# Optimization experiments

Hardware: AMD Instinct MI355X
Metric: run time of the kernel (lower is better)

Reference implementation:

```python
import jax, jax.numpy as jnp
import numpy as np

B, S, D = 2, 2048, 1024
H = 16
HD = D // H  # 64
FORESIGHT = -1e9  # masked_fill value for non-causal positions


def setup_inputs() -> dict:
    key = jax.random.key(0)
    ks = jax.random.split(key, 8)
    s = 0.02
    return {
        "x": jax.random.normal(ks[0], (B, S, D), dtype=jnp.float32),
        "Wq": jax.random.normal(ks[1], (D, H * HD), dtype=jnp.float32) * s,
        "bq": jax.random.normal(ks[2], (H * HD,), dtype=jnp.float32) * s,
        "Wk": jax.random.normal(ks[3], (D, H * HD), dtype=jnp.float32) * s,
        "Wv": jax.random.normal(ks[4], (D, H * HD), dtype=jnp.float32) * s,
        "Wo": jax.random.normal(ks[5], (H * HD, D), dtype=jnp.float32) * s,
        "bo": jax.random.normal(ks[6], (D,), dtype=jnp.float32) * s,
    }


def reference(x, Wq, bq, Wk, Wv, Wo, bo):
    b, s, _ = x.shape
    # projections -> [B, H, S, HD]
    q = (x @ Wq + bq).reshape(b, s, H, HD).transpose(0, 2, 1, 3)
    k = (x @ Wk).reshape(b, s, H, HD).transpose(0, 2, 1, 3)
    v = (x @ Wv).reshape(b, s, H, HD).transpose(0, 2, 1, 3)
    # scores [B, H, S, S]
    scores = jnp.einsum("bhqd,bhkd->bhqk", q, k) / jnp.sqrt(jnp.float32(HD))
    # ALiBi bias: slope_h * j (key position), broadcast over queries
    slopes = 2.0 ** (-8.0 * jnp.arange(1, H + 1, dtype=jnp.float32) / H)
    positions = jnp.arange(s, dtype=jnp.float32)
    scores = scores - slopes[None, :, None, None] * positions[None, None, None, :]
    # causal mask: fill strictly-upper triangle with foresight
    causal = jnp.tril(jnp.ones((s, s), dtype=bool))
    scores = jnp.where(causal[None, None, :, :], scores, FORESIGHT)
    attn = jax.nn.softmax(scores, axis=-1)
    out = jnp.einsum("bhqk,bhkd->bhqd", attn, v)
    out = out.transpose(0, 2, 1, 3).reshape(b, s, H * HD)
    return out @ Wo + bo
```

## Files before the change

### kernel.cpp

```cpp
#include <hip/hip_runtime.h>
#include <stdint.h>

#define DDIM 1024
#define HH 16
#define HDIM 64
#define SS 2048

typedef short bf16x8 __attribute__((ext_vector_type(8)));
typedef float f32x4 __attribute__((ext_vector_type(4)));
typedef float f32x16 __attribute__((ext_vector_type(16)));
typedef unsigned short u16;

__device__ __forceinline__ unsigned f2bf(float f) {
  unsigned u = __builtin_bit_cast(unsigned, f);
  u = u + 0x7FFFu + ((u >> 16) & 1u);
  return u >> 16;
}

__device__ __forceinline__ unsigned cvt_pk_bf16(float a, float b) {
  unsigned r;
  asm("v_cvt_pk_bf16_f32 %0, %1, %2" : "=v"(r) : "v"(a), "v"(b));
  return r;
}

__device__ __forceinline__ void pswap(unsigned& a, unsigned& b) {
  asm volatile("v_permlane32_swap_b32 %0, %1" : "+v"(a), "+v"(b));
}

__device__ __forceinline__ void gload16(const void* g, void* l) {
  __builtin_amdgcn_global_load_lds(
      (const __attribute__((address_space(1))) unsigned int*)g,
      (__attribute__((address_space(3))) unsigned int*)l, 16, 0, 0);
}

__device__ __forceinline__ f32x16 zero16() {
  f32x16 z;
#pragma unroll
  for (int r = 0; r < 16; r++) z[r] = 0.f;
  return z;
}

__global__ void k_convert_x(const float* __restrict__ x, u16* __restrict__ xb) {
  int i = (blockIdx.x * 256 + threadIdx.x) * 4;
  float4 v = *(const float4*)(x + i);
  ushort4 o;
  o.x = (u16)f2bf(v.x); o.y = (u16)f2bf(v.y); o.z = (u16)f2bf(v.z); o.w = (u16)f2bf(v.w);
  *(ushort4*)(xb + i) = o;
}

__global__ void k_transpose_w(const float* __restrict__ w0, const float* __restrict__ w1,
                              const float* __restrict__ w2, const float* __restrict__ w3,
                              u16* __restrict__ wt) {
  __shared__ float t[64][65];
  int z = blockIdx.z;
  const float* src = (z == 0) ? w0 : (z == 1) ? w1 : (z == 2) ? w2 : w3;
  u16* dst = wt + (size_t)z * DDIM * DDIM;
  int k0 = blockIdx.x * 64, n0 = blockIdx.y * 64;
  int tid = threadIdx.x;
  int c4 = tid & 15, rr = tid >> 4;
  for (int rep = 0; rep < 4; rep++) {
    int r = rr + rep * 16;
    float4 v = *(const float4*)(src + (size_t)(k0 + r) * DDIM + n0 + c4 * 4);
    t[r][c4 * 4 + 0] = v.x; t[r][c4 * 4 + 1] = v.y;
    t[r][c4 * 4 + 2] = v.z; t[r][c4 * 4 + 3] = v.w;
  }
  __syncthreads();
  for (int rep = 0; rep < 4; rep++) {
    int n = rr + rep * 16;
    ushort4 o;
    o.x = (u16)f2bf(t[c4 * 4 + 0][n]); o.y = (u16)f2bf(t[c4 * 4 + 1][n]);
    o.z = (u16)f2bf(t[c4 * 4 + 2][n]); o.w = (u16)f2bf(t[c4 * 4 + 3][n]);
    *(ushort4*)(dst + (size_t)(n0 + n) * DDIM + k0 + c4 * 4) = o;
  }
}

template <int MODE>
__global__ __launch_bounds__(256, 2) void k_gemm(const u16* __restrict__ A,
                                                 const u16* __restrict__ BT,
                                                 const float* __restrict__ bias,
                                                 void* __restrict__ O0,
                                                 void* __restrict__ O1,
                                                 void* __restrict__ O2) {
  __shared__ __align__(16) u16 lA[128 * 64];
  __shared__ __align__(16) u16 lB[128 * 64];
  const int tid = threadIdx.x;
  const int l = tid & 63, w = tid >> 6;
  const int wm = w >> 1, wn = w & 1;
  const int m0 = blockIdx.x * 128, n0 = blockIdx.y * 128;
  const int lr = l >> 4, lc = l & 15;

  const int srow = l >> 3;
  const int scol = ((l & 7) ^ srow) * 8;

  f32x4 acc[4][4];
  for (int mi = 0; mi < 4; mi++)
    for (int ni = 0; ni < 4; ni++)
      acc[mi][ni] = f32x4{0.f, 0.f, 0.f, 0.f};

  for (int kk = 0; kk < 16; kk++) {
    const int k0 = kk * 64;
    for (int i = 0; i < 4; i++) {
      int c = w * 4 + i;
      gload16(A + (size_t)(m0 + c * 8 + srow) * DDIM + k0 + scol, (char*)lA + c * 1024);
      gload16(BT + (size_t)(n0 + c * 8 + srow) * DDIM + k0 + scol, (char*)lB + c * 1024);
    }
    __syncthreads();
    for (int ks = 0; ks < 2; ks++) {
      bf16x8 af[4], bfr[4];
      for (int mi = 0; mi < 4; mi++) {
        int row = wm * 64 + mi * 16 + lc;
        int slot = (ks * 4 + lr) ^ (row & 7);
        af[mi] = *(const bf16x8*)((const char*)lA + row * 128 + slot * 16);
      }
      for (int ni = 0; ni < 4; ni++) {
        int row = wn * 64 + ni * 16 + lc;
        int slot = (ks * 4 + lr) ^ (row & 7);
        bfr[ni] = *(const bf16x8*)((const char*)lB + row * 128 + slot * 16);
      }
      for (int mi = 0; mi < 4; mi++)
        for (int ni = 0; ni < 4; ni++)
          acc[mi][ni] = __builtin_amdgcn_mfma_f32_16x16x32_bf16(af[mi], bfr[ni], acc[mi][ni], 0, 0, 0);
    }
    __syncthreads();
  }

  if (MODE == 0) {
    const int which = blockIdx.y >> 3;
    if (which == 0) {
      u16* C = (u16*)O0;
      const float c1 = 0.18033688011112043f;
      for (int mi = 0; mi < 4; mi++)
        for (int ni = 0; ni < 4; ni++) {
          int nl = (n0 + wn * 64 + ni * 16 + lc) & 1023;
          float badd = bias[nl];
          for (int r = 0; r < 4; r++) {
            int m = m0 + wm * 64 + mi * 16 + lr * 4 + r;
            C[(size_t)m * DDIM + nl] = (u16)f2bf((acc[mi][ni][r] + badd) * c1);
          }
        }
    } else if (which == 1) {
      u16* C = (u16*)O1;
      for (int mi = 0; mi < 4; mi++)
        for (int ni = 0; ni < 4; ni++) {
          int nl = (n0 + wn * 64 + ni * 16 + lc) & 1023;
          for (int r = 0; r < 4; r++) {
            int m = m0 + wm * 64 + mi * 16 + lr * 4 + r;
            C[(size_t)m * DDIM + nl] = (u16)f2bf(acc[mi][ni][r]);
          }
        }
    } else {
      u16* C = (u16*)O2;
      for (int mi = 0; mi < 4; mi++)
        for (int ni = 0; ni < 4; ni++) {
          int nl = (n0 + wn * 64 + ni * 16 + lc) & 1023;
          int h = nl >> 6, hd = nl & 63;
          int m = m0 + wm * 64 + mi * 16 + lr * 4;
          int b = m >> 11, s = m & 2047;
          unsigned d0 = f2bf(acc[mi][ni][0]) | (f2bf(acc[mi][ni][1]) << 16);
          unsigned d1 = f2bf(acc[mi][ni][2]) | (f2bf(acc[mi][ni][3]) << 16);
          u16* p = C + ((size_t)((b * HH + h) * HDIM + hd)) * SS + s;
          *(unsigned*)(p) = d0;
          *(unsigned*)(p + 2) = d1;
        }
    }
  } else {
    float* C = (float*)O0;
    for (int mi = 0; mi < 4; mi++)
      for (int ni = 0; ni < 4; ni++) {
        int n = n0 + wn * 64 + ni * 16 + lc;
        float badd = bias[n];
        for (int r = 0; r < 4; r++) {
          int m = m0 + wm * 64 + mi * 16 + lr * 4 + r;
          C[(size_t)m * DDIM + n] = acc[mi][ni][r] + badd;
        }
      }
  }
}

__global__ __launch_bounds__(256, 2) void k_attn(const u16* __restrict__ Q,
                                                 const u16* __restrict__ Kg,
                                                 const u16* __restrict__ Vt,
                                                 u16* __restrict__ AO) {
  __shared__ __align__(16) u16 lK[2][64 * 64];
  __shared__ __align__(16) u16 lV[2][64 * 64];

  const int tid = threadIdx.x;
  const int l = tid & 63, w = tid >> 6;
  const int lq = l & 31, hi = l >> 5;
  const int id = blockIdx.x;
  const int bh = id & 31;
  const int gslot = id >> 5;
  const int g = (gslot < 8) ? gslot : 23 - gslot;
  const int b = bh >> 4, h = bh & 15;
  const int sw = g * 4 + w;
  const int qglob = sw * 32 + lq;
  const int nktw = (sw >> 1) + 1;
  const int nkt = 2 * g + 2;

  const float slope2 = exp2f(-0.5f * (float)(h + 1)) * 1.4426950408889634f;
  const float sh4 = slope2 * (float)(4 * hi);

  f32x16 scr;
#pragma unroll
  for (int r = 0; r < 16; r++) scr[r] = slope2 * (float)((r & 3) + 8 * (r >> 2));

  bf16x8 qf[4];
#pragma unroll
  for (int sd = 0; sd < 4; sd++)
    qf[sd] = *(const bf16x8*)(Q + (size_t)(b * SS + qglob) * DDIM + h * HDIM + sd * 16 + hi * 8);

  f32x16 o0 = zero16(), o1 = zero16();
  float mrun = -3.0e38f, lrl = 0.f;

  const int srow = l >> 3;
  const int scol = ((l & 7) ^ srow) * 8;

  auto stage = [&](int kt, int bb) {
#pragma unroll
    for (int i = 0; i < 2; i++) {
      int c = i * 4 + w;
      gload16(Kg + (size_t)(b * SS + kt * 64 + c * 8 + srow) * DDIM + h * HDIM + scol,
              (char*)lK[bb] + c * 1024);
      gload16(Vt + ((size_t)bh * HDIM + c * 8 + srow) * SS + kt * 64 + scol,
              (char*)lV[bb] + c * 1024);
    }
  };

  stage(0, 0);
  stage(1, 1);

  for (int t = 0; t < nkt; t++) {
    asm volatile("s_waitcnt vmcnt(4)" ::: "memory");
    __builtin_amdgcn_s_barrier();
    asm volatile("" ::: "memory");
    if (t < nktw) {
      const char* Kc = (const char*)lK[t & 1];
      const char* Vc = (const char*)lV[t & 1];
      const bool lastp = (t == nktw - 1);
      const bool doT1 = !lastp || (sw & 1);
      const bool mT0 = lastp && !(sw & 1);
      const bool mT1 = lastp && (sw & 1);

      f32x16 s0 = zero16(), s1 = zero16();
      __builtin_amdgcn_s_setprio(1);
#pragma unroll
      for (int sd = 0; sd < 4; sd++) {
        int row = lq;
        int slot = (2 * sd + hi) ^ (row & 7);
        bf16x8 a = *(const bf16x8*)(Kc + row * 128 + slot * 16);
        s0 = __builtin_amdgcn_mfma_f32_32x32x16_bf16(a, qf[sd], s0, 0, 0, 0);
      }
      if (doT1) {
#pragma unroll
        for (int sd = 0; sd < 4; sd++) {
          int row = 32 + lq;
          int slot = (2 * sd + hi) ^ (row & 7);
          bf16x8 a = *(const bf16x8*)(Kc + row * 128 + slot * 16);
          s1 = __builtin_amdgcn_mfma_f32_32x32x16_bf16(a, qf[sd], s1, 0, 0, 0);
        }
      }
      __builtin_amdgcn_s_setprio(0);

      const float bt0 = -slope2 * (float)(t * 64) - sh4;
      const float bt1 = bt0 - slope2 * 32.f;
      float tmax = -3.0e38f;
#pragma unroll
      for (int r = 0; r < 16; r++) {
        float sv = (s0[r] + bt0) - scr[r];
        if (mT0) {
          int key = t * 64 + (r & 3) + 8 * (r >> 2) + 4 * hi;
          if (key > qglob) sv = -3.0e38f;
        }
        s0[r] = sv;
        tmax = fmaxf(tmax, sv);
      }
      if (doT1) {
#pragma unroll
        for (int r = 0; r < 16; r++) {
          float sv = (s1[r] + bt1) - scr[r];
          if (mT1) {
            int key = t * 64 + 32 + (r & 3) + 8 * (r >> 2) + 4 * hi;
            if (key > qglob) sv = -3.0e38f;
          }
          s1[r] = sv;
          tmax = fmaxf(tmax, sv);
        }
      }
      float tcol = fmaxf(tmax, __shfl_xor(tmax, 32));
      if (__any(tcol > mrun)) {
        float mnew = fmaxf(mrun, tcol);
        float corr = exp2f(mrun - mnew);
        lrl *= corr;
#pragma unroll
        for (int r = 0; r < 16; r++) { o0[r] *= corr; o1[r] *= corr; }
        mrun = mnew;
      }

      f32x4 ps = f32x4{0.f, 0.f, 0.f, 0.f};
#pragma unroll
      for (int r = 0; r < 16; r++) {
        float p = exp2f(s0[r] - mrun);
        s0[r] = p;
        ps[r & 3] += p;
      }
      if (doT1) {
#pragma unroll
        for (int r = 0; r < 16; r++) {
          float p = exp2f(s1[r] - mrun);
          s1[r] = p;
          ps[r & 3] += p;
        }
      }
      lrl += (ps[0] + ps[1]) + (ps[2] + ps[3]);

      __builtin_amdgcn_s_setprio(1);
      auto pvstep = [&](const f32x16& cs, int s) {
        const int b8 = (s & 1) * 8;
        unsigned x1 = cvt_pk_bf16(cs[b8 + 0], cs[b8 + 1]);
        unsigned y1 = cvt_pk_bf16(cs[b8 + 4], cs[b8 + 5]);
        pswap(x1, y1);
        unsigned x2 = cvt_pk_bf16(cs[b8 + 2], cs[b8 + 3]);
        unsigned y2 = cvt_pk_bf16(cs[b8 + 6], cs[b8 + 7]);
        pswap(x2, y2);
        uint4 pw; pw.x = x1; pw.y = x2; pw.z = y1; pw.w = y2;
        bf16x8 pb = __builtin_bit_cast(bf16x8, pw);
        int slotb = 2 * s + hi;
        {
          int row = lq;
          bf16x8 va = *(const bf16x8*)(Vc + row * 128 + ((slotb ^ (row & 7)) << 4));
          o0 = __builtin_amdgcn_mfma_f32_32x32x16_bf16(va, pb, o0, 0, 0, 0);
        }
        {
          int row = 32 + lq;
          bf16x8 va = *(const bf16x8*)(Vc + row * 128 + ((slotb ^ (row & 7)) << 4));
          o1 = __builtin_amdgcn_mfma_f32_32x32x16_bf16(va, pb, o1, 0, 0, 0);
        }
      };
      pvstep(s0, 0);
      pvstep(s0, 1);
      if (doT1) {
        pvstep(s1, 2);
        pvstep(s1, 3);
      }
      __builtin_amdgcn_s_setprio(0);
    }
    __builtin_amdgcn_s_barrier();
    asm volatile("" ::: "memory");
    int kts = t + 2;
    if (kts > nkt - 1) kts = nkt - 1;
    stage(kts, t & 1);
  }

  float lcol = lrl + __shfl_xor(lrl, 32);
  float inv = 1.f / lcol;
  u16* obase = AO + (size_t)(b * SS + qglob) * DDIM + h * HDIM;
#pragma unroll
  for (int rg = 0; rg < 4; rg++) {
    uint2 uu;
    uu.x = cvt_pk_bf16(o0[4 * rg + 0] * inv, o0[4 * rg + 1] * inv);
    uu.y = cvt_pk_bf16(o0[4 * rg + 2] * inv, o0[4 * rg + 3] * inv);
    *(uint2*)(obase + rg * 8 + 4 * hi) = uu;
    uu.x = cvt_pk_bf16(o1[4 * rg + 0] * inv, o1[4 * rg + 1] * inv);
    uu.y = cvt_pk_bf16(o1[4 * rg + 2] * inv, o1[4 * rg + 3] * inv);
    *(uint2*)(obase + 32 + rg * 8 + 4 * hi) = uu;
  }
}

extern "C" void kernel_launch(void* const* d_in, const int* in_sizes, int n_in,
                              void* d_out, int out_size, void* d_ws, size_t ws_size,
                              hipStream_t stream) {
  const float* x  = (const float*)d_in[0];
  const float* Wq = (const float*)d_in[1];
  const float* bq = (const float*)d_in[2];
  const float* Wk = (const float*)d_in[3];
  const float* Wv = (const float*)d_in[4];
  const float* Wo = (const float*)d_in[5];
  const float* bo = (const float*)d_in[6];
  float* out = (float*)d_out;

  u16* ws = (u16*)d_ws;
  const size_t MEG = 1024 * 1024;
  u16* xb = ws;
  u16* WT = ws + 4 * MEG;
  u16* Qb = ws + 8 * MEG;
  u16* Kb = ws + 12 * MEG;
  u16* Vt = ws + 16 * MEG;
  u16* AO = ws + 20 * MEG;

  k_convert_x<<<dim3(4096), dim3(256), 0, stream>>>(x, xb);
  k_transpose_w<<<dim3(16, 16, 4), dim3(256), 0, stream>>>(Wq, Wk, Wv, Wo, WT);
  k_gemm<0><<<dim3(32, 24), dim3(256), 0, stream>>>(xb, WT, bq, (void*)Qb, (void*)Kb, (void*)Vt);
  k_attn<<<dim3(512), dim3(256), 0, stream>>>(Qb, Kb, Vt, AO);
  k_gemm<1><<<dim3(32, 8), dim3(256), 0, stream>>>(AO, WT + 3 * MEG, bo, (void*)out, nullptr, nullptr);
}
```

Measured before the change: 133.6 us.

## Split causal attention along keys into chunks with a separate combine kernel

Attention blocks now each cover one 128-query tile and a chunk of at most eight key tiles, giving 1280 blocks in place of 512 paired blocks. Each block writes its unnormalized fp32 partial output plus running max and sum, and a new combine kernel merges the chunks with rescaled weights before writing bf16. The aim is to balance work across the GPU's compute units and improve occupancy under the causal triangle. The cost is an extra kernel launch, fp32 partial traffic to global memory, and a loop that decodes the block index.

```diff
diff --git a/kernel.cpp b/kernel.cpp
--- a/kernel.cpp
+++ b/kernel.cpp
@@ -177,10 +177,11 @@
   }
 }
 
-__global__ __launch_bounds__(256, 2) void k_attn(const u16* __restrict__ Q,
+__global__ __launch_bounds__(256, 5) void k_attn(const u16* __restrict__ Q,
                                                  const u16* __restrict__ Kg,
                                                  const u16* __restrict__ Vt,
-                                                 u16* __restrict__ AO) {
+                                                 float* __restrict__ Opart,
+                                                 float* __restrict__ Ml) {
   __shared__ __align__(16) u16 lK[2][64 * 64];
   __shared__ __align__(16) u16 lV[2][64 * 64];
 
@@ -189,13 +190,15 @@
   const int lq = l & 31, hi = l >> 5;
   const int id = blockIdx.x;
   const int bh = id & 31;
-  const int gslot = id >> 5;
-  const int g = (gslot < 8) ? gslot : 23 - gslot;
+  int rem = id >> 5, j = 0;
+  while (rem >= 1 + (j >> 2)) { rem -= 1 + (j >> 2); j++; }
+  const int c = rem;
   const int b = bh >> 4, h = bh & 15;
-  const int sw = g * 4 + w;
-  const int qglob = sw * 32 + lq;
-  const int nktw = (sw >> 1) + 1;
-  const int nkt = 2 * g + 2;
+  const int nkt_blk = 2 * j + 2;
+  const int t0 = c * 8;
+  const int t1 = min(t0 + 8, nkt_blk);
+  const int nktw = 2 * j + 1 + (w >> 1);
+  const int qglob = j * 128 + w * 32 + lq;
 
   const float slope2 = exp2f(-0.5f * (float)(h + 1)) * 1.4426950408889634f;
   const float sh4 = slope2 * (float)(4 * hi);
@@ -218,18 +221,18 @@
   auto stage = [&](int kt, int bb) {
 #pragma unroll
     for (int i = 0; i < 2; i++) {
-      int c = i * 4 + w;
-      gload16(Kg + (size_t)(b * SS + kt * 64 + c * 8 + srow) * DDIM + h * HDIM + scol,
-              (char*)lK[bb] + c * 1024);
-      gload16(Vt + ((size_t)bh * HDIM + c * 8 + srow) * SS + kt * 64 + scol,
-              (char*)lV[bb] + c * 1024);
+      int cc = i * 4 + w;
+      gload16(Kg + (size_t)(b * SS + kt * 64 + cc * 8 + srow) * DDIM + h * HDIM + scol,
+              (char*)lK[bb] + cc * 1024);
+      gload16(Vt + ((size_t)bh * HDIM + cc * 8 + srow) * SS + kt * 64 + scol,
+              (char*)lV[bb] + cc * 1024);
     }
   };
 
-  stage(0, 0);
-  stage(1, 1);
-
-  for (int t = 0; t < nkt; t++) {
+  stage(t0, 0);
+  stage(t0 + 1 < t1 ? t0 + 1 : t1 - 1, 1);
+
+  for (int t = t0; t < t1; t++) {
     asm volatile("s_waitcnt vmcnt(4)" ::: "memory");
     __builtin_amdgcn_s_barrier();
     asm volatile("" ::: "memory");
@@ -237,9 +240,9 @@
       const char* Kc = (const char*)lK[t & 1];
       const char* Vc = (const char*)lV[t & 1];
       const bool lastp = (t == nktw - 1);
-      const bool doT1 = !lastp || (sw & 1);
-      const bool mT0 = lastp && !(sw & 1);
-      const bool mT1 = lastp && (sw & 1);
+      const bool doT1 = !lastp || (w & 1);
+      const bool mT0 = lastp && !(w & 1);
+      const bool mT1 = lastp && (w & 1);
 
       f32x16 s0 = zero16(), s1 = zero16();
       __builtin_amdgcn_s_setprio(1);
@@ -347,23 +350,85 @@
     __builtin_amdgcn_s_barrier();
     asm volatile("" ::: "memory");
     int kts = t + 2;
-    if (kts > nkt - 1) kts = nkt - 1;
+    if (kts > t1 - 1) kts = t1 - 1;
     stage(kts, t & 1);
   }
 
   float lcol = lrl + __shfl_xor(lrl, 32);
-  float inv = 1.f / lcol;
-  u16* obase = AO + (size_t)(b * SS + qglob) * DDIM + h * HDIM;
+  float* Op = Opart + (size_t)id * 8192 + (w * 32 + lq) * 64;
 #pragma unroll
   for (int rg = 0; rg < 4; rg++) {
-    uint2 uu;
-    uu.x = cvt_pk_bf16(o0[4 * rg + 0] * inv, o0[4 * rg + 1] * inv);
-    uu.y = cvt_pk_bf16(o0[4 * rg + 2] * inv, o0[4 * rg + 3] * inv);
-    *(uint2*)(obase + rg * 8 + 4 * hi) = uu;
-    uu.x = cvt_pk_bf16(o1[4 * rg + 0] * inv, o1[4 * rg + 1] * inv);
-    uu.y = cvt_pk_bf16(o1[4 * rg + 2] * inv, o1[4 * rg + 3] * inv);
-    *(uint2*)(obase + 32 + rg * 8 + 4 * hi) = uu;
-  }
+    float4 v;
+    v.x = o0[4 * rg + 0]; v.y = o0[4 * rg + 1]; v.z = o0[4 * rg + 2]; v.w = o0[4 * rg + 3];
+    *(float4*)(Op + rg * 8 + 4 * hi) = v;
+    v.x = o1[4 * rg + 0]; v.y = o1[4 * rg + 1]; v.z = o1[4 * rg + 2]; v.w = o1[4 * rg + 3];
+    *(float4*)(Op + 32 + rg * 8 + 4 * hi) = v;
+  }
+  if (hi == 0) {
+    float2 mlv; mlv.x = mrun; mlv.y = lcol;
+    *(float2*)(Ml + (size_t)id * 256 + (w * 32 + lq) * 2) = mlv;
+  }
+}
+
+__global__ __launch_bounds__(256, 4) void k_combine(const float* __restrict__ Opart,
+                                                    const float* __restrict__ Ml,
+                                                    u16* __restrict__ AO) {
+  const int blk = blockIdx.x;
+  const int bh = blk & 31, qt = blk >> 5;
+  const int b = bh >> 4, h = bh & 15;
+  const int j = qt >> 1, g = j >> 2;
+  const int nc = g + 1;
+  const int base = 2 * g * (g + 1) + (j & 3) * (g + 1);
+  const int tid = threadIdx.x;
+  const int q = tid >> 2, seg = (tid & 3) << 4;
+  const int q128 = (qt & 1) * 64 + q;
+
+  float m0 = -3.0e38f, m1 = -3.0e38f, m2 = -3.0e38f, m3 = -3.0e38f;
+  float l0 = 0.f, l1 = 0.f, l2 = 0.f, l3 = 0.f;
+#pragma unroll 4
+  for (int cc = 0; cc < 4; cc++) {
+    if (cc >= nc) continue;
+    int sid = (base + cc) * 32 + bh;
+    float2 mlv = *(const float2*)(Ml + (size_t)sid * 256 + q128 * 2);
+    if (cc == 0) { m0 = mlv.x; l0 = mlv.y; }
+    else if (cc == 1) { m1 = mlv.x; l1 = mlv.y; }
+    else if (cc == 2) { m2 = mlv.x; l2 = mlv.y; }
+    else { m3 = mlv.x; l3 = mlv.y; }
+  }
+  float mstar = fmaxf(fmaxf(m0, m1), fmaxf(m2, m3));
+  float s0 = exp2f(m0 - mstar), s1 = exp2f(m1 - mstar);
+  float s2 = exp2f(m2 - mstar), s3 = exp2f(m3 - mstar);
+
+  float acc[16];
+#pragma unroll
+  for (int r = 0; r < 16; r++) acc[r] = 0.f;
+  float lstar = 0.f;
+#pragma unroll 4
+  for (int cc = 0; cc < 4; cc++) {
+    if (cc >= nc) continue;
+    float sc = (cc == 0) ? s0 : (cc == 1) ? s1 : (cc == 2) ? s2 : s3;
+    lstar += ((cc == 0) ? l0 : (cc == 1) ? l1 : (cc == 2) ? l2 : l3) * sc;
+    int sid = (base + cc) * 32 + bh;
+    const float* Op = Opart + (size_t)sid * 8192 + q128 * 64 + seg;
+#pragma unroll
+    for (int r4 = 0; r4 < 4; r4++) {
+      float4 v = *(const float4*)(Op + r4 * 4);
+      acc[r4 * 4 + 0] += v.x * sc;
+      acc[r4 * 4 + 1] += v.y * sc;
+      acc[r4 * 4 + 2] += v.z * sc;
+      acc[r4 * 4 + 3] += v.w * sc;
+    }
+  }
+  float inv = 1.f / lstar;
+  unsigned pk[8];
+#pragma unroll
+  for (int i = 0; i < 8; i++)
+    pk[i] = f2bf(acc[2 * i] * inv) | (f2bf(acc[2 * i + 1] * inv) << 16);
+  u16* ab = AO + (size_t)(b * SS + qt * 64 + q) * DDIM + h * HDIM + seg;
+  uint4 w0; w0.x = pk[0]; w0.y = pk[1]; w0.z = pk[2]; w0.w = pk[3];
+  uint4 w1; w1.x = pk[4]; w1.y = pk[5]; w1.z = pk[6]; w1.w = pk[7];
+  *(uint4*)(ab) = w0;
+  *(uint4*)(ab + 8) = w1;
 }
 
 extern "C" void kernel_launch(void* const* d_in, const int* in_sizes, int n_in,
@@ -386,10 +451,13 @@
   u16* Kb = ws + 12 * MEG;
   u16* Vt = ws + 16 * MEG;
   u16* AO = ws + 20 * MEG;
+  float* Opart = (float*)(ws + 24 * MEG);
+  float* Ml    = Opart + (size_t)1280 * 8192;
 
   k_convert_x<<<dim3(4096), dim3(256), 0, stream>>>(x, xb);
   k_transpose_w<<<dim3(16, 16, 4), dim3(256), 0, stream>>>(Wq, Wk, Wv, Wo, WT);
   k_gemm<0><<<dim3(32, 24), dim3(256), 0, stream>>>(xb, WT, bq, (void*)Qb, (void*)Kb, (void*)Vt);
-  k_attn<<<dim3(512), dim3(256), 0, stream>>>(Qb, Kb, Vt, AO);
+  k_attn<<<dim3(1280), dim3(256), 0, stream>>>(Qb, Kb, Vt, Opart, Ml);
+  k_combine<<<dim3(1024), dim3(256), 0, stream>>>(Opart, Ml, AO);
   k_gemm<1><<<dim3(32, 8), dim3(256), 0, stream>>>(AO, WT + 3 * MEG, bo, (void*)out, nullptr, nullptr);
 }
```

New measurement: 162.4 us. 21.5% more time.
